# Kernel optimization log

Measured on AMD Instinct MI355X. Metric: run time of the kernel, lower is better.

The kernel has to match this reference:

```python
import jax, jax.numpy as jnp
import numpy as np

B, C, H, W = 2, 3, 512, 512
P = 16
D = 768
NH = 12
DEPTH = 12
MLP = 4
HP, WP = H // P, W // P
N = HP * WP
DH = D // NH          # 64
ROPE_BASE = 100.0     # from pos_embed='RoPE100'


def _ln(x, w, b, eps):
    m = jnp.mean(x, -1, keepdims=True)
    v = jnp.mean((x - m) ** 2, -1, keepdims=True)
    return (x - m) * jax.lax.rsqrt(v + eps) * w + b


def _rope_tables(maxpos, d):
    inv = 1.0 / (ROPE_BASE ** (jnp.arange(0, d, 2, dtype=jnp.float32) / d))
    f = jnp.arange(maxpos, dtype=jnp.float32)[:, None] * inv[None, :]
    f = jnp.concatenate([f, f], -1)  # [maxpos, d]
    return jnp.cos(f), jnp.sin(f)


def _rot_half(x):
    x1, x2 = jnp.split(x, 2, -1)
    return jnp.concatenate([-x2, x1], -1)


def _rope2d(t, pos, cos, sin):
    # t: [B,NH,N,DH]; pos: [B,N,2] (y,x). First half of DH rotated by y, second by x.
    def rot1d(tok, p):
        c = cos[p][:, None]  # [B,1,N,DH//2]
        s = sin[p][:, None]
        return tok * c + _rot_half(tok) * s
    ty, tx = jnp.split(t, 2, -1)
    return jnp.concatenate([rot1d(ty, pos[..., 0]), rot1d(tx, pos[..., 1])], -1)


def _forward(image, patch_w, patch_b, ln1_w, ln1_b, qkv_w, qkv_b, proj_w, proj_b,
             ln2_w, ln2_b, fc1_w, fc1_b, fc2_w, fc2_b, encn_w, encn_b):
    # patch embed: conv stride=patch, flatten row-major (y-major, matching cartesian_prod(y,x))
    x = jax.lax.conv_general_dilated(image, patch_w, (P, P), 'VALID',
                                     dimension_numbers=('NCHW', 'OIHW', 'NCHW'))
    x = (x + patch_b[None, :, None, None]).reshape(B, D, N).transpose(0, 2, 1)  # [B,N,D]
    yy, xx = jnp.meshgrid(jnp.arange(HP), jnp.arange(WP), indexing='ij')
    pos = jnp.broadcast_to(jnp.stack([yy, xx], -1).reshape(N, 2), (B, N, 2))
    cos, sin = _rope_tables(max(HP, WP), DH // 2)
    scale = DH ** -0.5
    for i in range(DEPTH):
        h = _ln(x, ln1_w[i], ln1_b[i], 1e-5)
        qkv = (h @ qkv_w[i].T + qkv_b[i]).reshape(B, N, 3, NH, DH).transpose(2, 0, 3, 1, 4)
        q, k, v = qkv[0], qkv[1], qkv[2]  # [B,NH,N,DH]
        q = _rope2d(q, pos, cos, sin)
        k = _rope2d(k, pos, cos, sin)
        att = jax.nn.softmax(jnp.einsum('bhqd,bhkd->bhqk', q, k) * scale, -1)
        o = jnp.einsum('bhqk,bhkd->bhqd', att, v).transpose(0, 2, 1, 3).reshape(B, N, D)
        x = x + o @ proj_w[i].T + proj_b[i]
        h = _ln(x, ln2_w[i], ln2_b[i], 1e-5)
        h = jax.nn.gelu(h @ fc1_w[i].T + fc1_b[i], approximate=False)
        x = x + h @ fc2_w[i].T + fc2_b[i]
    x = _ln(x, encn_w, encn_b, 1e-6)
    return x, pos


def setup_inputs() -> dict:
    key = jax.random.key(0)
    ks = jax.random.split(key, 8)
    s = 0.02
    dff = MLP * D
    return {
        "image": jax.random.normal(ks[0], (B, C, H, W), jnp.float32),
        "true_shape": jnp.full((B, 2), H, jnp.int32),
        "patch_w": jax.random.normal(ks[1], (D, C, P, P), jnp.float32) * s,
        "patch_b": jnp.zeros((D,), jnp.float32),
        "ln1_w": jnp.ones((DEPTH, D), jnp.float32),
        "ln1_b": jnp.zeros((DEPTH, D), jnp.float32),
        "qkv_w": jax.random.normal(ks[2], (DEPTH, 3 * D, D), jnp.float32) * s,
        "qkv_b": jnp.zeros((DEPTH, 3 * D), jnp.float32),
        "proj_w": jax.random.normal(ks[3], (DEPTH, D, D), jnp.float32) * s,
        "proj_b": jnp.zeros((DEPTH, D), jnp.float32),
        "ln2_w": jnp.ones((DEPTH, D), jnp.float32),
        "ln2_b": jnp.zeros((DEPTH, D), jnp.float32),
        "fc1_w": jax.random.normal(ks[4], (DEPTH, dff, D), jnp.float32) * s,
        "fc1_b": jnp.zeros((DEPTH, dff), jnp.float32),
        "fc2_w": jax.random.normal(ks[5], (DEPTH, D, dff), jnp.float32) * s,
        "fc2_b": jnp.zeros((DEPTH, D), jnp.float32),
        "encn_w": jnp.ones((D,), jnp.float32),
        "encn_b": jnp.zeros((D,), jnp.float32),
    }


def reference(image, true_shape, patch_w, patch_b, ln1_w, ln1_b, qkv_w, qkv_b,
              proj_w, proj_b, ln2_w, ln2_b, fc1_w, fc1_b, fc2_w, fc2_b,
              encn_w, encn_b):
    # true_shape assumed full-resolution (all images H x W); positions are static grid
    return _forward(image, patch_w, patch_b, ln1_w, ln1_b, qkv_w, qkv_b, proj_w,
                    proj_b, ln2_w, ln2_b, fc1_w, fc1_b, fc2_w, fc2_b, encn_w, encn_b)
```

## Files before the change

kernel.cpp:

```cpp
#include <hip/hip_runtime.h>
#include <hip/hip_bf16.h>
#include <stdint.h>

typedef unsigned short u16;
typedef __attribute__((ext_vector_type(8))) short bf16x8;
typedef __attribute__((ext_vector_type(4))) float f32x4;
typedef __attribute__((ext_vector_type(4))) u16 u16x4;
typedef __attribute__((ext_vector_type(4))) uint32_t u32x4;

__device__ __forceinline__ u16 f2bf(float f) {
  union { float f; uint32_t u; } v; v.f = f;
  uint32_t u = v.u + 0x7FFFu + ((v.u >> 16) & 1u);
  return (u16)(u >> 16);
}
__device__ __forceinline__ float bf2f(u16 h) {
  union { uint32_t u; float f; } v; v.u = ((uint32_t)h) << 16;
  return v.f;
}

__device__ __forceinline__ int xcd_swz(int hw, int n) {
  return (n & 7) ? hw : (hw & 7) * (n >> 3) + (hw >> 3);
}

__device__ __forceinline__ void gload_lds16(const void* g, void* l) {
  __builtin_amdgcn_global_load_lds(
      (const __attribute__((address_space(1))) void*)g,
      (__attribute__((address_space(3))) void*)l, 16, 0, 0);
}

__global__ __launch_bounds__(256) void cast_f32_bf16(const float* __restrict__ src,
                                                     u16* __restrict__ dst, int n4) {
  int i = blockIdx.x * 256 + threadIdx.x;
  if (i < n4) {
    float4 v = ((const float4*)src)[i];
    u16x4 o; o.x = f2bf(v.x); o.y = f2bf(v.y); o.z = f2bf(v.z); o.w = f2bf(v.w);
    ((u16x4*)dst)[i] = o;
  }
}

__global__ __launch_bounds__(256) void im2col_kernel(const float* __restrict__ img,
                                                     u16* __restrict__ out) {
  int f = blockIdx.x * 256 + threadIdx.x;
  int row = blockIdx.y;
  int b = row >> 10, n = row & 1023, py = n >> 5, px = n & 31;
  int c = f >> 8, rem = f & 255, i = rem >> 4, j = rem & 15;
  float v = img[(((size_t)b * 3 + c) * 512 + py * 16 + i) * 512 + px * 16 + j];
  out[(size_t)row * 768 + f] = f2bf(v);
}

template <int EPI>
__global__ __launch_bounds__(256, 2)
void gemm_bt(const u16* __restrict__ A, const u16* __restrict__ W,
             const float* __restrict__ bias, void* __restrict__ outp,
             int M, int N, int K, int lda, int ldw) {
  constexpr int AB = 128 * 128;
  constexpr int BB = 128 * 128;
  constexpr int BUF = AB + BB;
  constexpr int LOADS = BUF / 4096;
  __shared__ char smem[2 * BUF];
  const int tid = threadIdx.x;
  const int lane = tid & 63;
  const int w = tid >> 6;
  const int qr = lane & 15;
  const int kg = lane >> 4;
  const int gx = gridDim.x;
  const int lid = xcd_swz(blockIdx.x + blockIdx.y * gx, gx * gridDim.y);
  const int bn = lid % gx, bm = lid / gx;
  const int wr = (w >> 1) * 64;
  const int wc = (w & 1) * 64;
  const size_t arow0 = (size_t)bm * 128;
  const size_t wrow0 = (size_t)bn * 128;
  const u16* Ab = A + (size_t)blockIdx.z * K;
  const u16* Wb = W + (size_t)blockIdx.z * K;

  f32x4 acc[4][4] = {};

  auto stage = [&](int buf, int kt) {
    char* As = smem + buf * BUF;
    char* Ws = As + AB;
#pragma unroll
    for (int r = 0; r < 4; ++r) {
      int o = r * 4096 + tid * 16;
      int row = o >> 7;
      int lc = (o & 127) ^ ((row & 7) << 4);
      gload_lds16(Ab + (arow0 + row) * lda + kt + (lc >> 1), As + o);
    }
#pragma unroll
    for (int r = 0; r < 4; ++r) {
      int o = r * 4096 + tid * 16;
      int row = o >> 7;
      int lc = (o & 127) ^ ((row & 7) << 4);
      gload_lds16(Wb + (wrow0 + row) * ldw + kt + (lc >> 1), Ws + o);
    }
  };

  const int nt = K >> 6;
  stage(0, 0);
  stage(1, 64);
  for (int t = 0; t < nt; ++t) {
    if (t + 1 < nt) {
      asm volatile("s_waitcnt vmcnt(%0)" :: "i"(LOADS) : "memory");
    } else {
      asm volatile("s_waitcnt vmcnt(0)" ::: "memory");
    }
    __builtin_amdgcn_s_barrier();
    const char* As = smem + (t & 1) * BUF;
    const char* Ws = As + AB;
    bf16x8 af[2][4], bfr[2][4];
#pragma unroll
    for (int ks = 0; ks < 2; ++ks) {
#pragma unroll
      for (int m = 0; m < 4; ++m) {
        int row = wr + m * 16 + qr;
        af[ks][m] = *(const bf16x8*)(As + row * 128 + ((ks * 64 + kg * 16) ^ ((row & 7) << 4)));
      }
#pragma unroll
      for (int n = 0; n < 4; ++n) {
        int row = wc + n * 16 + qr;
        bfr[ks][n] = *(const bf16x8*)(Ws + row * 128 + ((ks * 64 + kg * 16) ^ ((row & 7) << 4)));
      }
    }
    asm volatile("s_waitcnt lgkmcnt(0)" ::: "memory");
    __builtin_amdgcn_s_barrier();
    if (t + 2 < nt) stage(t & 1, (t + 2) << 6);
#pragma unroll
    for (int ks = 0; ks < 2; ++ks)
#pragma unroll
      for (int m = 0; m < 4; ++m)
#pragma unroll
        for (int n = 0; n < 4; ++n)
          acc[m][n] = __builtin_amdgcn_mfma_f32_16x16x32_bf16(af[ks][m], bfr[ks][n], acc[m][n], 0, 0, 0);
  }

  const int r0 = bm * 128 + wr + kg * 4;
  const int c0 = bn * 128 + wc + qr;
  if constexpr (EPI == 4) {
    const int headbase = bn * 128 + wc;
    const bool isqk = headbase < 1536;
    const float linv = exp2f(-0.41524101186092122f * (float)qr);
    u16* outb = (u16*)outp;
#pragma unroll
    for (int m = 0; m < 4; ++m) {
#pragma unroll
      for (int j = 0; j < 4; ++j) {
        int row = r0 + m * 16 + j;
        int tok = row & 1023;
        float vs[4];
#pragma unroll
        for (int n = 0; n < 4; ++n) vs[n] = acc[m][n][j] + bias[c0 + n * 16];
        if (isqk) {
          float sy, cy, sx, cx;
          __sincosf((float)(tok >> 5) * linv, &sy, &cy);
          __sincosf((float)(tok & 31) * linv, &sx, &cx);
          float a0 = vs[0], a1 = vs[1], a2 = vs[2], a3 = vs[3];
          vs[0] = a0 * cy - a1 * sy;
          vs[1] = a1 * cy + a0 * sy;
          vs[2] = a2 * cx - a3 * sx;
          vs[3] = a3 * cx + a2 * sx;
        }
#pragma unroll
        for (int n = 0; n < 4; ++n)
          outb[(size_t)row * N + c0 + n * 16] = f2bf(vs[n]);
      }
    }
  } else if constexpr (EPI == 5) {
    u16* outb = (u16*)outp + (size_t)blockIdx.z * M * N;
#pragma unroll
    for (int m = 0; m < 4; ++m)
#pragma unroll
      for (int j = 0; j < 4; ++j) {
        int row = r0 + m * 16 + j;
#pragma unroll
        for (int n = 0; n < 4; ++n)
          outb[(size_t)row * N + c0 + n * 16] = f2bf(acc[m][n][j]);
      }
  } else {
    u16* outb = (u16*)outp;
#pragma unroll
    for (int m = 0; m < 4; ++m)
#pragma unroll
      for (int j = 0; j < 4; ++j) {
        int row = r0 + m * 16 + j;
#pragma unroll
        for (int n = 0; n < 4; ++n) {
          int col = c0 + n * 16;
          float v = acc[m][n][j] + bias[col];
          v = 0.5f * v * (1.0f + erff(v * 0.70710678118654752f));
          outb[(size_t)row * N + col] = f2bf(v);
        }
      }
  }
}

template <int FINAL>
__global__ __launch_bounds__(256)
void fuse_red_ln(const u16* __restrict__ parts, const float* __restrict__ bias,
                 const float* __restrict__ resid, float* __restrict__ xout,
                 void* __restrict__ lnout, const float* __restrict__ lw,
                 const float* __restrict__ lb, float eps) {
  if (FINAL && blockIdx.x >= 2048) {
    int i = (blockIdx.x - 2048) * 256 + threadIdx.x;
    if (i < 4096) {
      int c = i & 1, n = (i >> 1) & 1023;
      ((float*)lnout)[(size_t)2048 * 768 + i] = (float)(c ? (n & 31) : (n >> 5));
    }
    return;
  }
  const int row = blockIdx.x, t = threadIdx.x;
  constexpr size_t MN = (size_t)2048 * 768;
  const u16* p0 = parts + (size_t)row * 768;
  float v[3];
#pragma unroll
  for (int e = 0; e < 3; ++e) {
    int c = t + e * 256;
    float s = bf2f(p0[c]) + bf2f(p0[MN + c]) + bf2f(p0[2 * MN + c]) + bf2f(p0[3 * MN + c]) + bias[c];
    if (resid) s += resid[(size_t)row * 768 + c];
    v[e] = s;
    xout[(size_t)row * 768 + c] = s;
  }
  float s = v[0] + v[1] + v[2];
  float sq = v[0] * v[0] + v[1] * v[1] + v[2] * v[2];
#pragma unroll
  for (int m = 1; m < 64; m <<= 1) {
    s += __shfl_xor(s, m);
    sq += __shfl_xor(sq, m);
  }
  __shared__ float red[8];
  int wv = t >> 6;
  if ((t & 63) == 0) { red[wv] = s; red[4 + wv] = sq; }
  __syncthreads();
  s = red[0] + red[1] + red[2] + red[3];
  sq = red[4] + red[5] + red[6] + red[7];
  float mean = s * (1.0f / 768.0f);
  float var = sq * (1.0f / 768.0f) - mean * mean;
  float rstd = rsqrtf(var + eps);
#pragma unroll
  for (int e = 0; e < 3; ++e) {
    int c = t + e * 256;
    float val = (v[e] - mean) * rstd * lw[c] + lb[c];
    if (FINAL)
      ((float*)lnout)[(size_t)row * 768 + c] = val;
    else
      ((u16*)lnout)[(size_t)row * 768 + c] = f2bf(val);
  }
}

__global__ __launch_bounds__(256)
void attn_kernel(const u16* __restrict__ qkv, u16* __restrict__ o) {
  __shared__ char smem[32768];
  const int tid = threadIdx.x, lane = tid & 63, w = tid >> 6;
  const int qr = lane & 15, kg = lane >> 4;
  const bool kgodd = (kg & 1) != 0;
  const int lid = xcd_swz(blockIdx.x, gridDim.x);
  const int qb = lid & 15, bh = lid >> 4;
  const int b = bh / 12, h = bh % 12;
  const int qrow0 = qb * 64 + w * 16;
  const u16* kvb = qkv + (size_t)b * 1024 * 2304;

  bf16x8 aq[2];
  {
    const u16* qbase = qkv + ((size_t)(b * 1024 + qrow0 + qr)) * 2304 + h * 64;
    aq[0] = *(const bf16x8*)(qbase + kg * 8);
    aq[1] = *(const bf16x8*)(qbase + 32 + kg * 8);
#pragma unroll
    for (int r = 0; r < 2; ++r)
#pragma unroll
      for (int e = 0; e < 8; ++e)
        aq[r][e] = (short)f2bf(bf2f((u16)aq[r][e]) * 0.125f);
  }
  f32x4 oacc[4] = {};
  float lsum = 0.f;

  const int kvp = tid >> 3, dg = tid & 7;
  bf16x8 va, vb;
  auto issueV = [&](int kt) {
    const u16* vsrc = kvb + ((size_t)(kt * 64 + kvp * 2)) * 2304 + 1536 + h * 64 + dg * 8;
    va = *(const bf16x8*)vsrc;
    vb = *(const bf16x8*)(vsrc + 2304);
  };
  auto issueK = [&](int kt, int bsel) {
    char* Ks = smem + bsel * 8192;
#pragma unroll
    for (int r = 0; r < 2; ++r) {
      int off = r * 4096 + tid * 16;
      int kv = off >> 7;
      int db = (off ^ ((kv & 7) << 4)) & 127;
      gload_lds16(kvb + ((size_t)(kt * 64 + kv)) * 2304 + 768 + h * 64 + (db >> 1), Ks + off);
    }
  };
  auto writeV = [&](int bsel) {
    char* Vt = smem + 16384 + bsel * 8192;
#pragma unroll
    for (int j = 0; j < 8; ++j) {
      int d = dg * 8 + j;
      uint32_t pk = (uint32_t)(u16)va[j] | ((uint32_t)(u16)vb[j] << 16);
      *(uint32_t*)(Vt + ((d * 128 + kvp * 4) ^ (((dg ^ j) & 7) << 4))) = pk;
    }
  };

  issueV(0);
  issueK(0, 0);
  writeV(0);

  for (int kt = 0; kt < 16; ++kt) {
    const int c = kt & 1;
    asm volatile("s_waitcnt vmcnt(0) lgkmcnt(0)" ::: "memory");
    __builtin_amdgcn_s_barrier();
    if (kt + 1 < 16) { issueV(kt + 1); issueK(kt + 1, c ^ 1); }

    const char* Ks = smem + c * 8192;
    const char* Vt = smem + 16384 + c * 8192;

    f32x4 sa[4] = {};
    __builtin_amdgcn_s_setprio(1);
#pragma unroll
    for (int ks = 0; ks < 2; ++ks)
#pragma unroll
      for (int n = 0; n < 4; ++n) {
        int row = n * 16 + qr;
        bf16x8 bk = *(const bf16x8*)(Ks + ((row * 128 + ks * 64 + kg * 16) ^ ((row & 7) << 4)));
        sa[n] = __builtin_amdgcn_mfma_f32_16x16x32_bf16(bk, aq[ks], sa[n], 0, 0, 0);
      }
    __builtin_amdgcn_s_setprio(0);

    float pv[4][4];
    float ts = 0.f;
#pragma unroll
    for (int n = 0; n < 4; ++n)
#pragma unroll
      for (int j = 0; j < 4; ++j) {
        pv[n][j] = __expf(sa[n][j]);
        ts += pv[n][j];
      }
    lsum += ts;

    if (kt + 1 < 16) writeV(c ^ 1);

    uint32_t pk0[4], pk1[4];
#pragma unroll
    for (int n = 0; n < 4; ++n) {
      asm("v_cvt_pk_bf16_f32 %0, %1, %2" : "=v"(pk0[n]) : "v"(pv[n][0]), "v"(pv[n][1]));
      asm("v_cvt_pk_bf16_f32 %0, %1, %2" : "=v"(pk1[n]) : "v"(pv[n][2]), "v"(pv[n][3]));
    }

    bf16x8 pb[2];
#pragma unroll
    for (int ks = 0; ks < 2; ++ks) {
      uint32_t A0 = pk0[ks * 2], B0 = pk0[ks * 2 + 1];
      uint32_t A1 = pk1[ks * 2], B1 = pk1[ks * 2 + 1];
      asm("v_permlane32_swap_b32 %0, %1" : "+v"(A0), "+v"(B0));
      asm("v_permlane32_swap_b32 %0, %1" : "+v"(A1), "+v"(B1));
      uint32_t sA0 = (uint32_t)__shfl_xor((int)A0, 16);
      uint32_t sA1 = (uint32_t)__shfl_xor((int)A1, 16);
      uint32_t sB0 = (uint32_t)__shfl_xor((int)B0, 16);
      uint32_t sB1 = (uint32_t)__shfl_xor((int)B1, 16);
      u32x4 dd;
      dd.x = kgodd ? sB0 : A0;
      dd.y = kgodd ? sB1 : A1;
      dd.z = kgodd ? B0 : sA0;
      dd.w = kgodd ? B1 : sA1;
      pb[ks] = __builtin_bit_cast(bf16x8, dd);
    }

    __builtin_amdgcn_s_setprio(1);
#pragma unroll
    for (int ks = 0; ks < 2; ++ks)
#pragma unroll
      for (int n = 0; n < 4; ++n) {
        int d = n * 16 + qr;
        bf16x8 vf = *(const bf16x8*)(Vt + ((d * 128 + ks * 64 + kg * 16) ^ ((((d >> 3) ^ (d & 7)) & 7) << 4)));
        oacc[n] = __builtin_amdgcn_mfma_f32_16x16x32_bf16(vf, pb[ks], oacc[n], 0, 0, 0);
      }
    __builtin_amdgcn_s_setprio(0);
  }
  lsum += __shfl_xor(lsum, 16);
  lsum += __shfl_xor(lsum, 32);
  float inv = 1.0f / lsum;
  const size_t rowg = (size_t)(b * 1024 + qrow0 + qr);
#pragma unroll
  for (int n = 0; n < 4; ++n) {
    u16x4 ov;
#pragma unroll
    for (int j = 0; j < 4; ++j) ov[j] = f2bf(oacc[n][j] * inv);
    *(u16x4*)(o + rowg * 768 + h * 64 + n * 16 + kg * 4) = ov;
  }
}

extern "C" void kernel_launch(void* const* d_in, const int* in_sizes, int n_in,
                              void* d_out, int out_size, void* d_ws, size_t ws_size,
                              hipStream_t stream) {
  const float* image  = (const float*)d_in[0];
  const float* patch_w = (const float*)d_in[2];
  const float* patch_b = (const float*)d_in[3];
  const float* ln1_w = (const float*)d_in[4];
  const float* ln1_b = (const float*)d_in[5];
  const float* qkv_w = (const float*)d_in[6];
  const float* qkv_b = (const float*)d_in[7];
  const float* proj_w = (const float*)d_in[8];
  const float* proj_b = (const float*)d_in[9];
  const float* ln2_w = (const float*)d_in[10];
  const float* ln2_b = (const float*)d_in[11];
  const float* fc1_w = (const float*)d_in[12];
  const float* fc1_b = (const float*)d_in[13];
  const float* fc2_w = (const float*)d_in[14];
  const float* fc2_b = (const float*)d_in[15];
  const float* encn_w = (const float*)d_in[16];
  const float* encn_b = (const float*)d_in[17];

  char* ws = (char*)d_ws;
  size_t off = 0;
  auto alloc = [&](size_t bytes) {
    char* pr = ws + off;
    off += (bytes + 255) & ~(size_t)255;
    return pr;
  };

  float* x    = (float*)alloc((size_t)2048 * 768 * 4);
  u16* hbuf   = (u16*)alloc((size_t)2048 * 768 * 2);
  u16* qkvb   = (u16*)alloc((size_t)2048 * 2304 * 2);
  u16* obuf   = (u16*)alloc((size_t)2048 * 768 * 2);
  u16* h2     = (u16*)alloc((size_t)2048 * 3072 * 2);
  u16* wpb    = (u16*)alloc((size_t)768 * 768 * 2);
  u16* parts  = (u16*)alloc((size_t)4 * 2048 * 768 * 2);

  const size_t wq_n = (size_t)12 * 2304 * 768;
  const size_t wp_n = (size_t)12 * 768 * 768;
  const size_t w1_n = (size_t)12 * 3072 * 768;
  const size_t w2_n = (size_t)12 * 3072 * 768;
  bool upfront = (off + 2 * (wq_n + wp_n + w1_n + w2_n) + (1u << 20)) <= ws_size;

  u16 *wq, *wp, *w1, *w2;
  if (upfront) {
    wq = (u16*)alloc(wq_n * 2);
    wp = (u16*)alloc(wp_n * 2);
    w1 = (u16*)alloc(w1_n * 2);
    w2 = (u16*)alloc(w2_n * 2);
  } else {
    wq = (u16*)alloc((size_t)2304 * 768 * 2);
    wp = (u16*)alloc((size_t)768 * 768 * 2);
    w1 = (u16*)alloc((size_t)3072 * 768 * 2);
    w2 = (u16*)alloc((size_t)3072 * 768 * 2);
  }

  auto cast = [&](const float* s, u16* d, size_t n) {
    int n4 = (int)(n / 4);
    cast_f32_bf16<<<(n4 + 255) / 256, 256, 0, stream>>>(s, d, n4);
  };

  cast(patch_w, wpb, (size_t)768 * 768);
  if (upfront) {
    cast(qkv_w, wq, wq_n);
    cast(proj_w, wp, wp_n);
    cast(fc1_w, w1, w1_n);
    cast(fc2_w, w2, w2_n);
  }

  im2col_kernel<<<dim3(3, 2048), 256, 0, stream>>>(image, hbuf);
  gemm_bt<5><<<dim3(6, 16, 4), 256, 0, stream>>>(hbuf, wpb, nullptr, parts, 2048, 768, 192, 768, 768);
  fuse_red_ln<0><<<2048, 256, 0, stream>>>(parts, patch_b, nullptr, x, hbuf, ln1_w, ln1_b, 1e-5f);

  for (int L = 0; L < 12; ++L) {
    u16 *wqL, *wpL, *w1L, *w2L;
    if (upfront) {
      wqL = wq + (size_t)L * 2304 * 768;
      wpL = wp + (size_t)L * 768 * 768;
      w1L = w1 + (size_t)L * 3072 * 768;
      w2L = w2 + (size_t)L * 3072 * 768;
    } else {
      cast(qkv_w + (size_t)L * 2304 * 768, wq, (size_t)2304 * 768);
      cast(proj_w + (size_t)L * 768 * 768, wp, (size_t)768 * 768);
      cast(fc1_w + (size_t)L * 3072 * 768, w1, (size_t)3072 * 768);
      cast(fc2_w + (size_t)L * 768 * 3072, w2, (size_t)3072 * 768);
      wqL = wq; wpL = wp; w1L = w1; w2L = w2;
    }
    gemm_bt<4><<<dim3(18, 16), 256, 0, stream>>>(hbuf, wqL, qkv_b + L * 2304, qkvb, 2048, 2304, 768, 768, 768);
    attn_kernel<<<384, 256, 0, stream>>>(qkvb, obuf);
    gemm_bt<5><<<dim3(6, 16, 4), 256, 0, stream>>>(obuf, wpL, nullptr, parts, 2048, 768, 192, 768, 768);
    fuse_red_ln<0><<<2048, 256, 0, stream>>>(parts, proj_b + L * 768, x, x, hbuf,
                                             ln2_w + L * 768, ln2_b + L * 768, 1e-5f);
    gemm_bt<1><<<dim3(24, 16), 256, 0, stream>>>(hbuf, w1L, fc1_b + L * 3072, h2, 2048, 3072, 768, 768, 768);
    gemm_bt<5><<<dim3(6, 16, 4), 256, 0, stream>>>(h2, w2L, nullptr, parts, 2048, 768, 768, 3072, 3072);
    if (L < 11) {
      fuse_red_ln<0><<<2048, 256, 0, stream>>>(parts, fc2_b + L * 768, x, x, hbuf,
                                               ln1_w + (L + 1) * 768, ln1_b + (L + 1) * 768, 1e-5f);
    } else {
      fuse_red_ln<1><<<2064, 256, 0, stream>>>(parts, fc2_b + L * 768, x, x, (float*)d_out,
                                               encn_w, encn_b, 1e-6f);
    }
  }
}
```

Before: 1.303 ms.

## Split LDS fragment loads around MFMAs, halve split-K, vectorize residual LayerNorm

In the GEMM main loop, the LDS fragment loads for the second k-slice are issued before the first slice's MFMAs, with partial lgkmcnt waits and sched barriers, so LDS latency overlaps matrix math. The attention kernel gets the same split for K fragment loads and hoists V fragment loads ahead of the P conversion. Split-K for the N=768 GEMMs drops from 4 to 2 partitions, which halves the partials buffer and the traffic the reduction reads. The reduce+LayerNorm kernel now uses 192 threads doing 4-wide vector loads and stores. The trade-off is fewer blocks (less parallelism) in the split-K GEMMs and more registers held live for the prefetched fragments.

```diff
diff --git a/kernel.cpp b/kernel.cpp
--- a/kernel.cpp
+++ b/kernel.cpp
@@ -108,28 +108,42 @@
     const char* Ws = As + AB;
     bf16x8 af[2][4], bfr[2][4];
 #pragma unroll
-    for (int ks = 0; ks < 2; ++ks) {
-#pragma unroll
-      for (int m = 0; m < 4; ++m) {
-        int row = wr + m * 16 + qr;
-        af[ks][m] = *(const bf16x8*)(As + row * 128 + ((ks * 64 + kg * 16) ^ ((row & 7) << 4)));
-      }
-#pragma unroll
-      for (int n = 0; n < 4; ++n) {
-        int row = wc + n * 16 + qr;
-        bfr[ks][n] = *(const bf16x8*)(Ws + row * 128 + ((ks * 64 + kg * 16) ^ ((row & 7) << 4)));
-      }
-    }
+    for (int m = 0; m < 4; ++m) {
+      int row = wr + m * 16 + qr;
+      af[0][m] = *(const bf16x8*)(As + row * 128 + ((kg * 16) ^ ((row & 7) << 4)));
+    }
+#pragma unroll
+    for (int n = 0; n < 4; ++n) {
+      int row = wc + n * 16 + qr;
+      bfr[0][n] = *(const bf16x8*)(Ws + row * 128 + ((kg * 16) ^ ((row & 7) << 4)));
+    }
+    __builtin_amdgcn_sched_barrier(0);
+#pragma unroll
+    for (int m = 0; m < 4; ++m) {
+      int row = wr + m * 16 + qr;
+      af[1][m] = *(const bf16x8*)(As + row * 128 + ((64 + kg * 16) ^ ((row & 7) << 4)));
+    }
+#pragma unroll
+    for (int n = 0; n < 4; ++n) {
+      int row = wc + n * 16 + qr;
+      bfr[1][n] = *(const bf16x8*)(Ws + row * 128 + ((64 + kg * 16) ^ ((row & 7) << 4)));
+    }
+    asm volatile("s_waitcnt lgkmcnt(8)" ::: "memory");
+    __builtin_amdgcn_sched_barrier(0);
+#pragma unroll
+    for (int m = 0; m < 4; ++m)
+#pragma unroll
+      for (int n = 0; n < 4; ++n)
+        acc[m][n] = __builtin_amdgcn_mfma_f32_16x16x32_bf16(af[0][m], bfr[0][n], acc[m][n], 0, 0, 0);
     asm volatile("s_waitcnt lgkmcnt(0)" ::: "memory");
+    __builtin_amdgcn_sched_barrier(0);
     __builtin_amdgcn_s_barrier();
     if (t + 2 < nt) stage(t & 1, (t + 2) << 6);
 #pragma unroll
-    for (int ks = 0; ks < 2; ++ks)
-#pragma unroll
-      for (int m = 0; m < 4; ++m)
-#pragma unroll
-        for (int n = 0; n < 4; ++n)
-          acc[m][n] = __builtin_amdgcn_mfma_f32_16x16x32_bf16(af[ks][m], bfr[ks][n], acc[m][n], 0, 0, 0);
+    for (int m = 0; m < 4; ++m)
+#pragma unroll
+      for (int n = 0; n < 4; ++n)
+        acc[m][n] = __builtin_amdgcn_mfma_f32_16x16x32_bf16(af[1][m], bfr[1][n], acc[m][n], 0, 0, 0);
   }
 
   const int r0 = bm * 128 + wr + kg * 4;
@@ -193,13 +207,13 @@
 }
 
 template <int FINAL>
-__global__ __launch_bounds__(256)
+__global__ __launch_bounds__(192)
 void fuse_red_ln(const u16* __restrict__ parts, const float* __restrict__ bias,
                  const float* __restrict__ resid, float* __restrict__ xout,
                  void* __restrict__ lnout, const float* __restrict__ lw,
                  const float* __restrict__ lb, float eps) {
   if (FINAL && blockIdx.x >= 2048) {
-    int i = (blockIdx.x - 2048) * 256 + threadIdx.x;
+    int i = (blockIdx.x - 2048) * 192 + threadIdx.x;
     if (i < 4096) {
       int c = i & 1, n = (i >> 1) & 1023;
       ((float*)lnout)[(size_t)2048 * 768 + i] = (float)(c ? (n & 31) : (n >> 5));
@@ -207,41 +221,44 @@
     return;
   }
   const int row = blockIdx.x, t = threadIdx.x;
+  const int c0 = t * 4;
   constexpr size_t MN = (size_t)2048 * 768;
-  const u16* p0 = parts + (size_t)row * 768;
-  float v[3];
-#pragma unroll
-  for (int e = 0; e < 3; ++e) {
-    int c = t + e * 256;
-    float s = bf2f(p0[c]) + bf2f(p0[MN + c]) + bf2f(p0[2 * MN + c]) + bf2f(p0[3 * MN + c]) + bias[c];
-    if (resid) s += resid[(size_t)row * 768 + c];
-    v[e] = s;
-    xout[(size_t)row * 768 + c] = s;
-  }
-  float s = v[0] + v[1] + v[2];
-  float sq = v[0] * v[0] + v[1] * v[1] + v[2] * v[2];
+  const u16x4 pa = *(const u16x4*)(parts + (size_t)row * 768 + c0);
+  const u16x4 pb = *(const u16x4*)(parts + MN + (size_t)row * 768 + c0);
+  const f32x4 bi = *(const f32x4*)(bias + c0);
+  f32x4 v;
+#pragma unroll
+  for (int j = 0; j < 4; ++j) v[j] = bf2f(pa[j]) + bf2f(pb[j]) + bi[j];
+  if (resid) v += *(const f32x4*)(resid + (size_t)row * 768 + c0);
+  *(f32x4*)(xout + (size_t)row * 768 + c0) = v;
+  float s = (v[0] + v[1]) + (v[2] + v[3]);
+  float sq = (v[0] * v[0] + v[1] * v[1]) + (v[2] * v[2] + v[3] * v[3]);
 #pragma unroll
   for (int m = 1; m < 64; m <<= 1) {
     s += __shfl_xor(s, m);
     sq += __shfl_xor(sq, m);
   }
-  __shared__ float red[8];
+  __shared__ float red[6];
   int wv = t >> 6;
-  if ((t & 63) == 0) { red[wv] = s; red[4 + wv] = sq; }
+  if ((t & 63) == 0) { red[wv] = s; red[3 + wv] = sq; }
   __syncthreads();
-  s = red[0] + red[1] + red[2] + red[3];
-  sq = red[4] + red[5] + red[6] + red[7];
+  s = red[0] + red[1] + red[2];
+  sq = red[3] + red[4] + red[5];
   float mean = s * (1.0f / 768.0f);
   float var = sq * (1.0f / 768.0f) - mean * mean;
   float rstd = rsqrtf(var + eps);
-#pragma unroll
-  for (int e = 0; e < 3; ++e) {
-    int c = t + e * 256;
-    float val = (v[e] - mean) * rstd * lw[c] + lb[c];
-    if (FINAL)
-      ((float*)lnout)[(size_t)row * 768 + c] = val;
-    else
-      ((u16*)lnout)[(size_t)row * 768 + c] = f2bf(val);
+  const f32x4 lwv = *(const f32x4*)(lw + c0);
+  const f32x4 lbv = *(const f32x4*)(lb + c0);
+  if (FINAL) {
+    f32x4 o;
+#pragma unroll
+    for (int j = 0; j < 4; ++j) o[j] = (v[j] - mean) * rstd * lwv[j] + lbv[j];
+    *(f32x4*)((float*)lnout + (size_t)row * 768 + c0) = o;
+  } else {
+    u16x4 o;
+#pragma unroll
+    for (int j = 0; j < 4; ++j) o[j] = f2bf((v[j] - mean) * rstd * lwv[j] + lbv[j]);
+    *(u16x4*)((u16*)lnout + (size_t)row * 768 + c0) = o;
   }
 }
 
@@ -311,16 +328,30 @@
     const char* Ks = smem + c * 8192;
     const char* Vt = smem + 16384 + c * 8192;
 
+    bf16x8 bk[2][4];
+#pragma unroll
+    for (int n = 0; n < 4; ++n) {
+      int row = n * 16 + qr;
+      bk[0][n] = *(const bf16x8*)(Ks + ((row * 128 + kg * 16) ^ ((row & 7) << 4)));
+    }
+    __builtin_amdgcn_sched_barrier(0);
+#pragma unroll
+    for (int n = 0; n < 4; ++n) {
+      int row = n * 16 + qr;
+      bk[1][n] = *(const bf16x8*)(Ks + ((row * 128 + 64 + kg * 16) ^ ((row & 7) << 4)));
+    }
     f32x4 sa[4] = {};
+    asm volatile("s_waitcnt lgkmcnt(4)" ::: "memory");
+    __builtin_amdgcn_sched_barrier(0);
     __builtin_amdgcn_s_setprio(1);
 #pragma unroll
-    for (int ks = 0; ks < 2; ++ks)
-#pragma unroll
-      for (int n = 0; n < 4; ++n) {
-        int row = n * 16 + qr;
-        bf16x8 bk = *(const bf16x8*)(Ks + ((row * 128 + ks * 64 + kg * 16) ^ ((row & 7) << 4)));
-        sa[n] = __builtin_amdgcn_mfma_f32_16x16x32_bf16(bk, aq[ks], sa[n], 0, 0, 0);
-      }
+    for (int n = 0; n < 4; ++n)
+      sa[n] = __builtin_amdgcn_mfma_f32_16x16x32_bf16(bk[0][n], aq[0], sa[n], 0, 0, 0);
+    asm volatile("s_waitcnt lgkmcnt(0)" ::: "memory");
+    __builtin_amdgcn_sched_barrier(0);
+#pragma unroll
+    for (int n = 0; n < 4; ++n)
+      sa[n] = __builtin_amdgcn_mfma_f32_16x16x32_bf16(bk[1][n], aq[1], sa[n], 0, 0, 0);
     __builtin_amdgcn_s_setprio(0);
 
     float pv[4][4];
@@ -336,13 +367,21 @@
 
     if (kt + 1 < 16) writeV(c ^ 1);
 
+    bf16x8 vf[2][4];
+#pragma unroll
+    for (int ks = 0; ks < 2; ++ks)
+#pragma unroll
+      for (int n = 0; n < 4; ++n) {
+        int d = n * 16 + qr;
+        vf[ks][n] = *(const bf16x8*)(Vt + ((d * 128 + ks * 64 + kg * 16) ^ ((((d >> 3) ^ (d & 7)) & 7) << 4)));
+      }
+
     uint32_t pk0[4], pk1[4];
 #pragma unroll
     for (int n = 0; n < 4; ++n) {
       asm("v_cvt_pk_bf16_f32 %0, %1, %2" : "=v"(pk0[n]) : "v"(pv[n][0]), "v"(pv[n][1]));
       asm("v_cvt_pk_bf16_f32 %0, %1, %2" : "=v"(pk1[n]) : "v"(pv[n][2]), "v"(pv[n][3]));
     }
-
     bf16x8 pb[2];
 #pragma unroll
     for (int ks = 0; ks < 2; ++ks) {
@@ -366,11 +405,8 @@
 #pragma unroll
     for (int ks = 0; ks < 2; ++ks)
 #pragma unroll
-      for (int n = 0; n < 4; ++n) {
-        int d = n * 16 + qr;
-        bf16x8 vf = *(const bf16x8*)(Vt + ((d * 128 + ks * 64 + kg * 16) ^ ((((d >> 3) ^ (d & 7)) & 7) << 4)));
-        oacc[n] = __builtin_amdgcn_mfma_f32_16x16x32_bf16(vf, pb[ks], oacc[n], 0, 0, 0);
-      }
+      for (int n = 0; n < 4; ++n)
+        oacc[n] = __builtin_amdgcn_mfma_f32_16x16x32_bf16(vf[ks][n], pb[ks], oacc[n], 0, 0, 0);
     __builtin_amdgcn_s_setprio(0);
   }
   lsum += __shfl_xor(lsum, 16);
@@ -421,7 +457,7 @@
   u16* obuf   = (u16*)alloc((size_t)2048 * 768 * 2);
   u16* h2     = (u16*)alloc((size_t)2048 * 3072 * 2);
   u16* wpb    = (u16*)alloc((size_t)768 * 768 * 2);
-  u16* parts  = (u16*)alloc((size_t)4 * 2048 * 768 * 2);
+  u16* parts  = (u16*)alloc((size_t)2 * 2048 * 768 * 2);
 
   const size_t wq_n = (size_t)12 * 2304 * 768;
   const size_t wp_n = (size_t)12 * 768 * 768;
@@ -456,8 +492,8 @@
   }
 
   im2col_kernel<<<dim3(3, 2048), 256, 0, stream>>>(image, hbuf);
-  gemm_bt<5><<<dim3(6, 16, 4), 256, 0, stream>>>(hbuf, wpb, nullptr, parts, 2048, 768, 192, 768, 768);
-  fuse_red_ln<0><<<2048, 256, 0, stream>>>(parts, patch_b, nullptr, x, hbuf, ln1_w, ln1_b, 1e-5f);
+  gemm_bt<5><<<dim3(6, 16, 2), 256, 0, stream>>>(hbuf, wpb, nullptr, parts, 2048, 768, 384, 768, 768);
+  fuse_red_ln<0><<<2048, 192, 0, stream>>>(parts, patch_b, nullptr, x, hbuf, ln1_w, ln1_b, 1e-5f);
 
   for (int L = 0; L < 12; ++L) {
     u16 *wqL, *wpL, *w1L, *w2L;
@@ -475,16 +511,16 @@
     }
     gemm_bt<4><<<dim3(18, 16), 256, 0, stream>>>(hbuf, wqL, qkv_b + L * 2304, qkvb, 2048, 2304, 768, 768, 768);
     attn_kernel<<<384, 256, 0, stream>>>(qkvb, obuf);
-    gemm_bt<5><<<dim3(6, 16, 4), 256, 0, stream>>>(obuf, wpL, nullptr, parts, 2048, 768, 192, 768, 768);
-    fuse_red_ln<0><<<2048, 256, 0, stream>>>(parts, proj_b + L * 768, x, x, hbuf,
+    gemm_bt<5><<<dim3(6, 16, 2), 256, 0, stream>>>(obuf, wpL, nullptr, parts, 2048, 768, 384, 768, 768);
+    fuse_red_ln<0><<<2048, 192, 0, stream>>>(parts, proj_b + L * 768, x, x, hbuf,
                                              ln2_w + L * 768, ln2_b + L * 768, 1e-5f);
     gemm_bt<1><<<dim3(24, 16), 256, 0, stream>>>(hbuf, w1L, fc1_b + L * 3072, h2, 2048, 3072, 768, 768, 768);
-    gemm_bt<5><<<dim3(6, 16, 4), 256, 0, stream>>>(h2, w2L, nullptr, parts, 2048, 768, 768, 3072, 3072);
+    gemm_bt<5><<<dim3(6, 16, 2), 256, 0, stream>>>(h2, w2L, nullptr, parts, 2048, 768, 1536, 3072, 3072);
     if (L < 11) {
-      fuse_red_ln<0><<<2048, 256, 0, stream>>>(parts, fc2_b + L * 768, x, x, hbuf,
+      fuse_red_ln<0><<<2048, 192, 0, stream>>>(parts, fc2_b + L * 768, x, x, hbuf,
                                                ln1_w + (L + 1) * 768, ln1_b + (L + 1) * 768, 1e-5f);
     } else {
-      fuse_red_ln<1><<<2064, 256, 0, stream>>>(parts, fc2_b + L * 768, x, x, (float*)d_out,
+      fuse_red_ln<1><<<2070, 192, 0, stream>>>(parts, fc2_b + L * 768, x, x, (float*)d_out,
                                                encn_w, encn_b, 1e-6f);
     }
   }
```

Result: no change. 1.281 ms (-1.7%).
